# Kernel tuning notes

Hardware: AMD Instinct MI355X
Metric: run time of the kernel (lower is better)

Reference implementation:

```python
import jax, jax.numpy as jnp
import numpy as np


def setup_inputs() -> dict:
    key = jax.random.key(0)
    ks = jax.random.split(key, 7)
    B, C, H, W = 8, 512, 32, 32
    N = 4
    Cn = C // N
    return {
        "first": jax.random.normal(ks[0], (B, C, H, W), dtype=jnp.float32),
        "second": jax.random.normal(ks[1], (B, C, H, W), dtype=jnp.float32),
        "w1": jax.random.normal(ks[2], (Cn, Cn), dtype=jnp.float32) * 0.05,
        "w2": jax.random.normal(ks[3], (Cn, Cn), dtype=jnp.float32) * 0.05,
        "w3": jax.random.normal(ks[4], (Cn, Cn), dtype=jnp.float32) * 0.05,
        "w4": jax.random.normal(ks[5], (Cn, Cn), dtype=jnp.float32) * 0.05,
        "w5": jax.random.normal(ks[6], (C, N), dtype=jnp.float32) * 0.05,
        "head_count": N,
    }


def reference(first, second, w1, w2, w3, w4, w5, head_count):
    B, C, H, W = first.shape
    N = head_count
    Cn = C // N
    L = H * W
    f = first.reshape(B * N, Cn, L)   # [BN, Cn, L]
    s = second.reshape(B * N, Cn, L)
    # 1x1 convs (no bias) == channel matmuls
    key_t = jnp.einsum('oc,bcl->blo', w1, f)    # [BN, L, Cn]
    query = jnp.einsum('oc,bcl->bol', w2, s)    # [BN, Cn, L]
    scores = jnp.einsum('blc,bcm->blm', key_t, query)  # [BN, L, L]
    attn = jax.nn.softmax(scores, axis=2)
    v1_t = jnp.einsum('oc,bcl->blo', w3, f)     # [BN, L, Cn]
    v2 = jnp.einsum('oc,bcl->bol', w4, s)       # [BN, Cn, L]
    value = jnp.einsum('blc,bcm->blm', v1_t, v2)  # [BN, L, L]
    res = jnp.sum(attn * value, axis=2)         # [BN, L]
    res = res.reshape(B, N, H, W)
    out = jax.nn.relu(jnp.einsum('on,bnhw->bohw', w5, res))  # [B, C, H, W]
    return out
```

## Files before the change

kernel.cpp:

```cpp
#include <hip/hip_runtime.h>
#include <hip/hip_bf16.h>
#include <stdint.h>

constexpr int BN = 32;
constexpr int Cn = 128;
constexpr int L  = 1024;
constexpr int CC = 512;
constexpr int BB = 8;

typedef __bf16 bf16x8 __attribute__((ext_vector_type(8)));
typedef float  f32x4  __attribute__((ext_vector_type(4)));
typedef unsigned short u16x8 __attribute__((ext_vector_type(8)));

__device__ inline unsigned short f2bf(float f) {
    unsigned int x = __float_as_uint(f);
    x += 0x7fffu + ((x >> 16) & 1u);
    return (unsigned short)(x >> 16);
}

__device__ inline void gl_lds16(const void* g, void* l) {
    typedef __attribute__((address_space(1))) const unsigned int GU;
    typedef __attribute__((address_space(3))) unsigned int LU;
    __builtin_amdgcn_global_load_lds((GU*)g, (LU*)l, 16, 0, 0);
}

__global__ __launch_bounds__(256)
void mkM_kernel(const float* __restrict__ w1, const float* __restrict__ w2,
                const float* __restrict__ w3, const float* __restrict__ w4,
                unsigned short* __restrict__ Mh, unsigned short* __restrict__ Ml)
{
    const int mb  = blockIdx.x;
    const int mat = mb >> 3;
    const int cq  = mb & 7;
    const int t   = threadIdx.x;
    const float* wa = mat ? w3 : w1;
    const float* wb = mat ? w4 : w2;
    const int c   = cq * 16 + (t & 15);
    const int cg2 = t >> 4;
    float acc[8];
    #pragma unroll
    for (int j = 0; j < 8; ++j) acc[j] = 0.f;
    for (int o = 0; o < 128; ++o) {
        float a = wa[o * 128 + c];
        #pragma unroll
        for (int j = 0; j < 8; ++j)
            acc[j] += a * wb[o * 128 + cg2 * 8 + j];
    }
    u16x8 hi, lo;
    #pragma unroll
    for (int j = 0; j < 8; ++j) {
        unsigned short h = f2bf(acc[j]);
        hi[j] = h;
        lo[j] = f2bf(acc[j] - __uint_as_float((unsigned)h << 16));
    }
    const int off = mat * 16384 + c * 128 + cg2 * 8;
    *(u16x8*)&Mh[off] = hi;
    *(u16x8*)&Ml[off] = lo;
}

__global__ __launch_bounds__(512)
void prep_kernel(const float* __restrict__ second,
                 const unsigned short* __restrict__ Mh,
                 const unsigned short* __restrict__ Ml,
                 unsigned short* __restrict__ Y1, unsigned short* __restrict__ Y2)
{
    __shared__ unsigned short shs[64 * 128];
    __shared__ unsigned short sls[64 * 128];
    __shared__ unsigned short yrep[2][64 * 128];

    const int p  = blockIdx.x;
    const int mt = p & 15;
    const int bn = p >> 4;

    const float* s = second + (size_t)bn * Cn * L + mt * 64;

    const int tid  = threadIdx.x;
    const int lane = tid & 63;
    const int wid  = tid >> 6;
    const int mat  = wid & 1;
    const int cq   = wid >> 1;
    const int r16  = lane & 15;
    const int g    = lane >> 4;

    const unsigned short* MHm = Mh + mat * 16384;
    const unsigned short* MLm = Ml + mat * 16384;

    bf16x8 mh[2][4], ml[2][4];
    #pragma unroll
    for (int og = 0; og < 2; ++og)
        #pragma unroll
        for (int kk = 0; kk < 4; ++kk) {
            int c  = cq * 32 + og * 16 + r16;
            int cp = kk * 32 + g * 8;
            mh[og][kk] = *(const bf16x8*)&MHm[c * 128 + cp];
            ml[og][kk] = *(const bf16x8*)&MLm[c * 128 + cp];
        }

    {
        const int sm   = tid & 63;
        const int cblk = tid >> 6;
        #pragma unroll
        for (int h = 0; h < 2; ++h) {
            const int chunk = cblk * 2 + h;
            const int c0 = chunk * 8;
            float v[8];
            #pragma unroll
            for (int j = 0; j < 8; ++j)
                v[j] = s[(size_t)(c0 + j) * L + sm];
            u16x8 hi, lo;
            #pragma unroll
            for (int j = 0; j < 8; ++j) {
                unsigned short hh = f2bf(v[j]);
                hi[j] = hh;
                lo[j] = f2bf(v[j] - __uint_as_float((unsigned)hh << 16));
            }
            const int off = sm * 128 + (chunk ^ (sm & 15)) * 8;
            *(u16x8*)&shs[off] = hi;
            *(u16x8*)&sls[off] = lo;
        }
    }
    __syncthreads();

    #pragma unroll
    for (int ms = 0; ms < 4; ++ms) {
        const int row = ms * 16 + r16;
        bf16x8 bh[4], bl[4];
        #pragma unroll
        for (int kk = 0; kk < 4; ++kk) {
            const int slot = ((kk << 2) + g) ^ r16;
            bh[kk] = *(const bf16x8*)&shs[row * 128 + slot * 8];
            bl[kk] = *(const bf16x8*)&sls[row * 128 + slot * 8];
        }
        f32x4 acc[2];
        acc[0] = (f32x4){0.f, 0.f, 0.f, 0.f};
        acc[1] = (f32x4){0.f, 0.f, 0.f, 0.f};
        #pragma unroll
        for (int kk = 0; kk < 4; ++kk)
            #pragma unroll
            for (int og = 0; og < 2; ++og) {
                f32x4 a = acc[og];
                a = __builtin_amdgcn_mfma_f32_16x16x32_bf16(mh[og][kk], bh[kk], a, 0, 0, 0);
                a = __builtin_amdgcn_mfma_f32_16x16x32_bf16(ml[og][kk], bh[kk], a, 0, 0, 0);
                a = __builtin_amdgcn_mfma_f32_16x16x32_bf16(mh[og][kk], bl[kk], a, 0, 0, 0);
                acc[og] = a;
            }
        const int m = ms * 16 + r16;
        #pragma unroll
        for (int og = 0; og < 2; ++og) {
            const int c0 = cq * 32 + og * 16 + g * 4;
            f32x4 a = acc[og];
            ushort4 st;
            st.x = f2bf(a.x); st.y = f2bf(a.y);
            st.z = f2bf(a.z); st.w = f2bf(a.w);
            const int pos = (((c0 >> 3) ^ (m & 7)) << 3) | (c0 & 7);
            *(ushort4*)&yrep[mat][m * 128 + pos] = st;
        }
    }
    __syncthreads();

    {
        unsigned short* Y1t = Y1 + (size_t)bn * (L * Cn) + mt * 8192;
        unsigned short* Y2t = Y2 + (size_t)bn * (L * Cn) + mt * 8192;
        #pragma unroll
        for (int i = 0; i < 2; ++i) {
            const int off = (i * 512 + tid) * 8;
            *(u16x8*)&Y1t[off] = *(const u16x8*)&yrep[0][off];
            *(u16x8*)&Y2t[off] = *(const u16x8*)&yrep[1][off];
        }
    }
}

__global__ __launch_bounds__(256, 2)
void attn_kernel(const float* __restrict__ first,
                 const unsigned short* __restrict__ Y1,
                 const unsigned short* __restrict__ Y2,
                 float* __restrict__ Dp, float* __restrict__ Rp)
{
    __shared__ char smem[2][32768];

    const int p   = blockIdx.x;
    const int xcd = p & 7;
    const int jj  = p >> 3;
    const int bn  = xcd * 4 + (jj & 3);
    const int lt  = (jj >> 2) & 3;
    const int mh  = jj >> 4;

    const int tid  = threadIdx.x;
    const int lane = tid & 63;
    const int w    = tid >> 6;
    const int r16  = lane & 15;
    const int g    = lane >> 4;
    const int swz  = lane & 7;

    const size_t slab = (size_t)L * Cn;
    const float* f = first + (size_t)bn * slab;
    const unsigned short* Q = Y1 + (size_t)bn * slab;
    const unsigned short* V = Y2 + (size_t)bn * slab;

    {
        unsigned short* fs = (unsigned short*)&smem[0][0];
        const int sl   = tid & 63;
        const int cblk = tid >> 6;
        #pragma unroll
        for (int lq = 0; lq < 4; ++lq) {
            const int ll = lq * 64 + sl;
            #pragma unroll
            for (int i = 0; i < 4; ++i) {
                const int chunk = cblk * 4 + i;
                const int c0 = chunk * 8;
                float v[8];
                #pragma unroll
                for (int j = 0; j < 8; ++j)
                    v[j] = f[(size_t)(c0 + j) * L + lt * 256 + ll];
                u16x8 hi;
                #pragma unroll
                for (int j = 0; j < 8; ++j) hi[j] = f2bf(v[j]);
                *(u16x8*)&fs[ll * 128 + (chunk ^ (ll & 15)) * 8] = hi;
            }
        }
    }
    __syncthreads();

    bf16x8 bf[4][4];
    {
        const unsigned short* fs = (const unsigned short*)&smem[0][0];
        #pragma unroll
        for (int st = 0; st < 4; ++st)
            #pragma unroll
            for (int kk = 0; kk < 4; ++kk) {
                const int row = (w * 4 + st) * 16 + r16;
                const int slot = ((kk << 2) + g) ^ r16;
                bf[st][kk] = *(const bf16x8*)&fs[row * 128 + slot * 8];
            }
    }
    __syncthreads();

    auto STAGE = [&](int buf, int t) {
        const int m0 = mh * 256 + t * 64;
        const char* qs = (const char*)Q + (size_t)m0 * 256;
        const char* vs = (const char*)V + (size_t)m0 * 256;
        char* qd = &smem[buf][0];
        char* vd = &smem[buf][16384];
        #pragma unroll
        for (int it = 0; it < 4; ++it) {
            gl_lds16(qs + tid * 16 + it * 4096, qd + tid * 16 + it * 4096);
            gl_lds16(vs + tid * 16 + it * 4096, vd + tid * 16 + it * 4096);
        }
    };

    STAGE(0, 0);
    __syncthreads();

    float Dacc[4] = {0.f, 0.f, 0.f, 0.f};
    float Racc[4] = {0.f, 0.f, 0.f, 0.f};
    const f32x4 z = {0.f, 0.f, 0.f, 0.f};

    for (int t = 0; t < 4; ++t) {
        const int buf = t & 1;
        if (t < 3) STAGE(buf ^ 1, t + 1);
        const char* qb = &smem[buf][0];
        const char* vb = &smem[buf][16384];
        #pragma unroll
        for (int mg = 0; mg < 4; ++mg) {
            const int brow = mg * 16 + r16;
            const int rbase = brow * 256;
            bf16x8 qf[4], vf[4];
            #pragma unroll
            for (int kk = 0; kk < 4; ++kk) {
                int off = rbase + ((((kk << 2) + g) ^ swz) << 4);
                qf[kk] = *(const bf16x8*)(qb + off);
                vf[kk] = *(const bf16x8*)(vb + off);
            }
            #pragma unroll
            for (int st = 0; st < 4; ++st) {
                f32x4 s0 = z, u0 = z;
                #pragma unroll
                for (int kk = 0; kk < 4; ++kk) {
                    s0 = __builtin_amdgcn_mfma_f32_16x16x32_bf16(qf[kk], bf[st][kk], s0, 0, 0, 0);
                    u0 = __builtin_amdgcn_mfma_f32_16x16x32_bf16(vf[kk], bf[st][kk], u0, 0, 0, 0);
                }
                float e0 = __expf(s0.x - 8.f);
                float e1 = __expf(s0.y - 8.f);
                float e2 = __expf(s0.z - 8.f);
                float e3 = __expf(s0.w - 8.f);
                Dacc[st] += (e0 + e1) + (e2 + e3);
                Racc[st] += (e0 * u0.x + e1 * u0.y) + (e2 * u0.z + e3 * u0.w);
            }
        }
        __syncthreads();
    }

    #pragma unroll
    for (int st = 0; st < 4; ++st) {
        Dacc[st] += __shfl_xor(Dacc[st], 16);
        Racc[st] += __shfl_xor(Racc[st], 16);
        Dacc[st] += __shfl_xor(Dacc[st], 32);
        Racc[st] += __shfl_xor(Racc[st], 32);
    }
    if (g == 0) {
        #pragma unroll
        for (int st = 0; st < 4; ++st) {
            const int l = lt * 256 + (w * 4 + st) * 16 + r16;
            size_t idx = (size_t)mh * BN * L + (size_t)bn * L + l;
            Dp[idx] = Dacc[st];
            Rp[idx] = Racc[st];
        }
    }
}

__global__ __launch_bounds__(256)
void combine_kernel(const float* __restrict__ Dp, const float* __restrict__ Rp,
                    float* __restrict__ res)
{
    int i = blockIdx.x * 256 + threadIdx.x;
    float d = Dp[i] + Dp[BN * L + i] + Dp[2 * BN * L + i] + Dp[3 * BN * L + i];
    float r = Rp[i] + Rp[BN * L + i] + Rp[2 * BN * L + i] + Rp[3 * BN * L + i];
    res[i] = r / d;
}

__global__ __launch_bounds__(256)
void out_kernel(const float* __restrict__ res, const float* __restrict__ w5,
                float* __restrict__ out)
{
    const int blk = blockIdx.x;
    const int o = blk & 511;
    const int b = blk >> 9;
    const float4 wv = *(const float4*)&w5[o * 4];

    const float* r0 = res + (size_t)(b * 4 + 0) * L;
    const float* r1 = res + (size_t)(b * 4 + 1) * L;
    const float* r2 = res + (size_t)(b * 4 + 2) * L;
    const float* r3 = res + (size_t)(b * 4 + 3) * L;

    const int hw = threadIdx.x * 4;
    float4 a0 = *(const float4*)&r0[hw];
    float4 a1 = *(const float4*)&r1[hw];
    float4 a2 = *(const float4*)&r2[hw];
    float4 a3 = *(const float4*)&r3[hw];

    float4 ov;
    ov.x = fmaxf(0.f, wv.x * a0.x + wv.y * a1.x + wv.z * a2.x + wv.w * a3.x);
    ov.y = fmaxf(0.f, wv.x * a0.y + wv.y * a1.y + wv.z * a2.y + wv.w * a3.y);
    ov.z = fmaxf(0.f, wv.x * a0.z + wv.y * a1.z + wv.z * a2.z + wv.w * a3.z);
    ov.w = fmaxf(0.f, wv.x * a0.w + wv.y * a1.w + wv.z * a2.w + wv.w * a3.w);

    *(float4*)&out[(size_t)blk * 1024 + hw] = ov;
}

extern "C" void kernel_launch(void* const* d_in, const int* in_sizes, int n_in,
                              void* d_out, int out_size, void* d_ws, size_t ws_size,
                              hipStream_t stream)
{
    const float* first  = (const float*)d_in[0];
    const float* second = (const float*)d_in[1];
    const float* w1 = (const float*)d_in[2];
    const float* w2 = (const float*)d_in[3];
    const float* w3 = (const float*)d_in[4];
    const float* w4 = (const float*)d_in[5];
    const float* w5 = (const float*)d_in[6];
    float* out = (float*)d_out;

    const size_t slabElems = (size_t)L * Cn;
    const size_t arr = (size_t)BN * slabElems;

    unsigned short* Y1 = (unsigned short*)d_ws;
    unsigned short* Y2 = Y1 + arr;
    unsigned short* Mh = Y2 + arr;
    unsigned short* Ml = Mh + 2 * 16384;
    float* Dp  = (float*)(Ml + 2 * 16384);
    float* Rp  = Dp + 4 * BN * L;
    float* res = Rp + 4 * BN * L;

    mkM_kernel<<<dim3(16), dim3(256), 0, stream>>>(w1, w2, w3, w4, Mh, Ml);
    prep_kernel<<<dim3(512), dim3(512), 0, stream>>>(second, Mh, Ml, Y1, Y2);
    attn_kernel<<<dim3(512), dim3(256), 0, stream>>>(first, Y1, Y2, Dp, Rp);
    combine_kernel<<<dim3(BN * L / 256), dim3(256), 0, stream>>>(Dp, Rp, res);
    out_kernel<<<dim3(BB * CC), dim3(256), 0, stream>>>(res, w5, out);
}
```

Measured before the change: 64.92 us.

## Stage fp32 inputs into LDS via direct global-to-LDS loads, convert on read

Both the prep and attention kernels now copy fp32 `second`/`first` tiles straight into shared memory using global_load_lds, replacing per-thread strided scalar global loads followed by register conversion. The bf16 hi/lo split now happens when fragments are read from LDS. The prep kernel tile doubles to 128 positions with half as many blocks, and the attention kernel loads its fp32 tile in two channel halves to fit the existing shared buffer. The aim is coalesced, asynchronous loads instead of uncoalesced strided ones. The cost is scalar strided LDS reads with possible bank conflicts, larger LDS use per prep block, and fewer prep blocks.

```diff
diff --git a/kernel.cpp b/kernel.cpp
--- a/kernel.cpp
+++ b/kernel.cpp
@@ -16,6 +16,9 @@
     unsigned int x = __float_as_uint(f);
     x += 0x7fffu + ((x >> 16) & 1u);
     return (unsigned short)(x >> 16);
+}
+__device__ inline __bf16 bfbits(unsigned short u) {
+    union { unsigned short s; __bf16 b; } cv; cv.s = u; return cv.b;
 }
 
 __device__ inline void gl_lds16(const void* g, void* l) {
@@ -64,15 +67,14 @@
                  const unsigned short* __restrict__ Ml,
                  unsigned short* __restrict__ Y1, unsigned short* __restrict__ Y2)
 {
-    __shared__ unsigned short shs[64 * 128];
-    __shared__ unsigned short sls[64 * 128];
-    __shared__ unsigned short yrep[2][64 * 128];
+    __shared__ float ss[128 * 128];
+    __shared__ unsigned short yrep[2][128 * 128];
 
     const int p  = blockIdx.x;
-    const int mt = p & 15;
-    const int bn = p >> 4;
-
-    const float* s = second + (size_t)bn * Cn * L + mt * 64;
+    const int mo = p & 7;
+    const int bn = p >> 3;
+
+    const float* s = second + (size_t)bn * Cn * L + mo * 128;
 
     const int tid  = threadIdx.x;
     const int lane = tid & 63;
@@ -85,6 +87,16 @@
     const unsigned short* MHm = Mh + mat * 16384;
     const unsigned short* MLm = Ml + mat * 16384;
 
+    {
+        const int row = tid >> 5;
+        const int m4  = (tid & 31) * 4;
+        #pragma unroll
+        for (int i = 0; i < 8; ++i) {
+            const int cr = i * 16 + row;
+            gl_lds16(s + (size_t)cr * L + m4, &ss[cr * 128 + m4]);
+        }
+    }
+
     bf16x8 mh[2][4], ml[2][4];
     #pragma unroll
     for (int og = 0; og < 2; ++og)
@@ -95,41 +107,21 @@
             mh[og][kk] = *(const bf16x8*)&MHm[c * 128 + cp];
             ml[og][kk] = *(const bf16x8*)&MLm[c * 128 + cp];
         }
-
-    {
-        const int sm   = tid & 63;
-        const int cblk = tid >> 6;
-        #pragma unroll
-        for (int h = 0; h < 2; ++h) {
-            const int chunk = cblk * 2 + h;
-            const int c0 = chunk * 8;
-            float v[8];
-            #pragma unroll
-            for (int j = 0; j < 8; ++j)
-                v[j] = s[(size_t)(c0 + j) * L + sm];
-            u16x8 hi, lo;
+    __syncthreads();
+
+    #pragma unroll
+    for (int ms = 0; ms < 8; ++ms) {
+        const int m = ms * 16 + r16;
+        bf16x8 bh[4], bl[4];
+        #pragma unroll
+        for (int kk = 0; kk < 4; ++kk) {
             #pragma unroll
             for (int j = 0; j < 8; ++j) {
-                unsigned short hh = f2bf(v[j]);
-                hi[j] = hh;
-                lo[j] = f2bf(v[j] - __uint_as_float((unsigned)hh << 16));
-            }
-            const int off = sm * 128 + (chunk ^ (sm & 15)) * 8;
-            *(u16x8*)&shs[off] = hi;
-            *(u16x8*)&sls[off] = lo;
-        }
-    }
-    __syncthreads();
-
-    #pragma unroll
-    for (int ms = 0; ms < 4; ++ms) {
-        const int row = ms * 16 + r16;
-        bf16x8 bh[4], bl[4];
-        #pragma unroll
-        for (int kk = 0; kk < 4; ++kk) {
-            const int slot = ((kk << 2) + g) ^ r16;
-            bh[kk] = *(const bf16x8*)&shs[row * 128 + slot * 8];
-            bl[kk] = *(const bf16x8*)&sls[row * 128 + slot * 8];
+                float v = ss[(kk * 32 + g * 8 + j) * 128 + m];
+                unsigned short h = f2bf(v);
+                bh[kk][j] = bfbits(h);
+                bl[kk][j] = bfbits(f2bf(v - __uint_as_float((unsigned)h << 16)));
+            }
         }
         f32x4 acc[2];
         acc[0] = (f32x4){0.f, 0.f, 0.f, 0.f};
@@ -144,7 +136,6 @@
                 a = __builtin_amdgcn_mfma_f32_16x16x32_bf16(mh[og][kk], bl[kk], a, 0, 0, 0);
                 acc[og] = a;
             }
-        const int m = ms * 16 + r16;
         #pragma unroll
         for (int og = 0; og < 2; ++og) {
             const int c0 = cq * 32 + og * 16 + g * 4;
@@ -159,10 +150,10 @@
     __syncthreads();
 
     {
-        unsigned short* Y1t = Y1 + (size_t)bn * (L * Cn) + mt * 8192;
-        unsigned short* Y2t = Y2 + (size_t)bn * (L * Cn) + mt * 8192;
-        #pragma unroll
-        for (int i = 0; i < 2; ++i) {
+        unsigned short* Y1t = Y1 + (size_t)bn * (L * Cn) + mo * 16384;
+        unsigned short* Y2t = Y2 + (size_t)bn * (L * Cn) + mo * 16384;
+        #pragma unroll
+        for (int i = 0; i < 4; ++i) {
             const int off = (i * 512 + tid) * 8;
             *(u16x8*)&Y1t[off] = *(const u16x8*)&yrep[0][off];
             *(u16x8*)&Y2t[off] = *(const u16x8*)&yrep[1][off];
@@ -197,43 +188,35 @@
     const unsigned short* Q = Y1 + (size_t)bn * slab;
     const unsigned short* V = Y2 + (size_t)bn * slab;
 
-    {
-        unsigned short* fs = (unsigned short*)&smem[0][0];
-        const int sl   = tid & 63;
-        const int cblk = tid >> 6;
-        #pragma unroll
-        for (int lq = 0; lq < 4; ++lq) {
-            const int ll = lq * 64 + sl;
-            #pragma unroll
-            for (int i = 0; i < 4; ++i) {
-                const int chunk = cblk * 4 + i;
-                const int c0 = chunk * 8;
-                float v[8];
+    bf16x8 bf[4][4];
+    float* fsf = (float*)&smem[0][0];
+    #pragma unroll
+    for (int half = 0; half < 2; ++half) {
+        {
+            const int row = tid >> 6;
+            const int l4  = (tid & 63) * 4;
+            #pragma unroll
+            for (int i = 0; i < 16; ++i) {
+                const int c = half * 64 + i * 4 + row;
+                gl_lds16(f + (size_t)c * L + lt * 256 + l4,
+                         &fsf[(i * 4 + row) * 256 + l4]);
+            }
+        }
+        __syncthreads();
+        #pragma unroll
+        for (int st = 0; st < 4; ++st)
+            #pragma unroll
+            for (int k2 = 0; k2 < 2; ++k2) {
+                const int kk = half * 2 + k2;
+                const int ll = (w * 4 + st) * 16 + r16;
                 #pragma unroll
-                for (int j = 0; j < 8; ++j)
-                    v[j] = f[(size_t)(c0 + j) * L + lt * 256 + ll];
-                u16x8 hi;
-                #pragma unroll
-                for (int j = 0; j < 8; ++j) hi[j] = f2bf(v[j]);
-                *(u16x8*)&fs[ll * 128 + (chunk ^ (ll & 15)) * 8] = hi;
-            }
-        }
-    }
-    __syncthreads();
-
-    bf16x8 bf[4][4];
-    {
-        const unsigned short* fs = (const unsigned short*)&smem[0][0];
-        #pragma unroll
-        for (int st = 0; st < 4; ++st)
-            #pragma unroll
-            for (int kk = 0; kk < 4; ++kk) {
-                const int row = (w * 4 + st) * 16 + r16;
-                const int slot = ((kk << 2) + g) ^ r16;
-                bf[st][kk] = *(const bf16x8*)&fs[row * 128 + slot * 8];
-            }
-    }
-    __syncthreads();
+                for (int j = 0; j < 8; ++j) {
+                    float v = fsf[(k2 * 32 + g * 8 + j) * 256 + ll];
+                    bf[st][kk][j] = bfbits(f2bf(v));
+                }
+            }
+        __syncthreads();
+    }
 
     auto STAGE = [&](int buf, int t) {
         const int m0 = mh * 256 + t * 64;
@@ -372,7 +355,7 @@
     float* res = Rp + 4 * BN * L;
 
     mkM_kernel<<<dim3(16), dim3(256), 0, stream>>>(w1, w2, w3, w4, Mh, Ml);
-    prep_kernel<<<dim3(512), dim3(512), 0, stream>>>(second, Mh, Ml, Y1, Y2);
+    prep_kernel<<<dim3(256), dim3(512), 0, stream>>>(second, Mh, Ml, Y1, Y2);
     attn_kernel<<<dim3(512), dim3(256), 0, stream>>>(first, Y1, Y2, Dp, Rp);
     combine_kernel<<<dim3(BN * L / 256), dim3(256), 0, stream>>>(Dp, Rp, res);
     out_kernel<<<dim3(BB * CC), dim3(256), 0, stream>>>(res, w5, out);
```

New measurement: 69.94 us. 1.08x slower.
